# Optimization experiments

Measured on AMD Instinct MI355X. Metric: run time of the kernel, lower is better.

The kernel has to match this reference:

```python
import jax, jax.numpy as jnp
import numpy as np

NUM_INST = 3
N_NODES = 50000
IN_F = 128
HID = 64
HEADS = 4
HF = HEADS * HID  # 256
NEG_SLOPE = 0.2
BN_EPS = 1e-5


def setup_inputs() -> dict:
    key = jax.random.key(0)
    ks = jax.random.split(key, 10)
    sppmi = jax.random.normal(ks[0], (NUM_INST, N_NODES, IN_F), dtype=jnp.float32)
    edge_index = jax.random.randint(ks[1], (2, 800000), 0, N_NODES, dtype=jnp.int64)
    # Per-instance GATConv params (lin_src weight, att_src/att_dst, bias), BN, and Linear
    s = 1.0 / np.sqrt(IN_F)
    W = jax.random.uniform(ks[2], (NUM_INST, HF, IN_F), jnp.float32, -s, s)
    att_src = jax.random.uniform(ks[3], (NUM_INST, HEADS, HID), jnp.float32, -s, s)
    att_dst = jax.random.uniform(ks[4], (NUM_INST, HEADS, HID), jnp.float32, -s, s)
    bias = jnp.zeros((NUM_INST, HF), jnp.float32)
    bn_gamma = jnp.ones((NUM_INST, HF), jnp.float32)
    bn_beta = jnp.zeros((NUM_INST, HF), jnp.float32)
    bn_mean = jnp.zeros((NUM_INST, HF), jnp.float32)
    bn_var = jnp.ones((NUM_INST, HF), jnp.float32)
    s2 = 1.0 / np.sqrt(HF)
    lin_W = jax.random.uniform(ks[5], (NUM_INST, HID, HF), jnp.float32, -s2, s2)
    lin_b = jax.random.uniform(ks[6], (NUM_INST, HID), jnp.float32, -s2, s2)
    return {"sppmi": sppmi, "W": W, "att_src": att_src, "att_dst": att_dst,
            "bias": bias, "bn_gamma": bn_gamma, "bn_beta": bn_beta,
            "bn_mean": bn_mean, "bn_var": bn_var, "lin_W": lin_W,
            "lin_b": lin_b, "edge_index": edge_index}


def _gat_layer(x, W, a_src, a_dst, bias, gamma, beta, mean, var, linW, linb, src, dst):
    # GATConv (concat=True, add_self_loops already applied via src/dst)
    xw = (x @ W.T).reshape(N_NODES, HEADS, HID)            # [N,H,F]
    alpha_src = (xw * a_src).sum(-1)                        # [N,H]
    alpha_dst = (xw * a_dst).sum(-1)                        # [N,H]
    e = jax.nn.leaky_relu(alpha_src[src] + alpha_dst[dst], NEG_SLOPE)  # [E,H]
    m = jax.ops.segment_max(e, dst, num_segments=N_NODES)  # segment softmax over dst
    e = jnp.exp(e - m[dst])
    denom = jax.ops.segment_sum(e, dst, num_segments=N_NODES)
    alpha = e / (denom[dst] + 1e-16)                        # [E,H]
    msg = alpha[:, :, None] * xw[src]                       # [E,H,F] gather-attend
    out = jax.ops.segment_sum(msg, dst, num_segments=N_NODES)  # scatter-add
    out = out.reshape(N_NODES, HF) + bias
    # BatchNorm1d (eval: running stats), ReLU, Linear
    out = (out - mean) * jax.lax.rsqrt(var + BN_EPS) * gamma + beta
    out = jax.nn.relu(out)
    return out @ linW.T + linb                              # [N,HID]


def reference(sppmi, W, att_src, att_dst, bias, bn_gamma, bn_beta, bn_mean, bn_var, lin_W, lin_b, edge_index):
    loop = jnp.arange(N_NODES, dtype=edge_index.dtype)
    src = jnp.concatenate([edge_index[0], loop])
    dst = jnp.concatenate([edge_index[1], loop])
    all_emb = jnp.zeros((N_NODES, HID), jnp.float32)
    for i in range(NUM_INST):
        all_emb = all_emb + _gat_layer(sppmi[i], W[i], att_src[i], att_dst[i], bias[i],
                                       bn_gamma[i], bn_beta[i], bn_mean[i], bn_var[i],
                                       lin_W[i], lin_b[i], src, dst)
    out_1 = all_emb / jnp.linalg.norm(all_emb, axis=1, keepdims=True)
    return out_1
```

## Files before the change

kernel.cpp:

```cpp
#include <hip/hip_runtime.h>
#include <hip/hip_bf16.h>

#define N_NODES 50000
#define E0      800000
#define ET      850000
#define IN_F    128
#define HF      256
#define HID     64
#define NEG     0.2f
#define BN_EPSC 1e-5f
#define NSCAN_BLK 196

typedef __attribute__((ext_vector_type(8))) short bh8;
typedef __attribute__((ext_vector_type(4))) float fl4;
typedef __attribute__((ext_vector_type(8))) unsigned short us8;

__device__ __forceinline__ float lrelu(float x){ return x > 0.f ? x : NEG * x; }
__device__ __forceinline__ unsigned short f2b(float f){
  unsigned int x = __float_as_uint(f);
  unsigned int r = x + 0x7FFF + ((x >> 16) & 1);
  return (unsigned short)(r >> 16);
}
__device__ __forceinline__ float b2f(unsigned short u){
  return __uint_as_float((unsigned int)u << 16);
}

__global__ __launch_bounds__(256) void k_cvt(const float* __restrict__ in,
                                             unsigned short* __restrict__ out, int n4){
  int i = blockIdx.x * 256 + threadIdx.x;
  int stride = gridDim.x * 256;
  for (; i < n4; i += stride){
    float4 v = ((const float4*)in)[i];
    ushort4 o;
    o.x = f2b(v.x); o.y = f2b(v.y); o.z = f2b(v.z); o.w = f2b(v.w);
    ((ushort4*)out)[i] = o;
  }
}

__global__ __launch_bounds__(256) void k_bnprep(const float* __restrict__ g, const float* __restrict__ b,
                                                const float* __restrict__ m, const float* __restrict__ v,
                                                float* __restrict__ scale, float* __restrict__ shiftv){
  int i = blockIdx.x * 256 + threadIdx.x;
  if (i >= 3 * HF) return;
  float s = g[i] * rsqrtf(v[i] + BN_EPSC);
  scale[i] = s;
  shiftv[i] = b[i] - m[i] * s;
}

__global__ void k_hist(const int* __restrict__ ei, int* __restrict__ counts){
  int e = blockIdx.x * 256 + threadIdx.x;
  if (e >= ET) return;
  int d = (e < E0) ? ei[E0 + e] : (e - E0);
  atomicAdd(&counts[d], 1);
}

__global__ __launch_bounds__(256) void k_bsum(const int* __restrict__ counts, int* __restrict__ bsums){
  int b = blockIdx.x;
  int t = threadIdx.x;
  int idx = b * 256 + t;
  int v = (idx < N_NODES) ? counts[idx] : 0;
  for (int m = 1; m < 64; m <<= 1) v += __shfl_xor(v, m, 64);
  __shared__ int ws[4];
  int lane = t & 63, w = t >> 6;
  if (lane == 0) ws[w] = v;
  __syncthreads();
  if (t == 0) bsums[b] = ws[0] + ws[1] + ws[2] + ws[3];
}

__global__ __launch_bounds__(256) void k_bscan(const int* __restrict__ bsums, int* __restrict__ bexcl,
                                               int* __restrict__ row_ptr){
  int t = threadIdx.x;
  int v = (t < NSCAN_BLK) ? bsums[t] : 0;
  int lane = t & 63, w = t >> 6;
  int incl = v;
  for (int m = 1; m < 64; m <<= 1){
    int n = __shfl_up(incl, m, 64);
    if (lane >= m) incl += n;
  }
  __shared__ int ws[4];
  if (lane == 63) ws[w] = incl;
  __syncthreads();
  if (t == 0){
    int r = 0;
    for (int j = 0; j < 4; ++j){ int x = ws[j]; ws[j] = r; r += x; }
  }
  __syncthreads();
  int excl = incl - v + ws[w];
  if (t < NSCAN_BLK) bexcl[t] = excl;
  if (t == 255) row_ptr[N_NODES] = excl + v;
}

__global__ __launch_bounds__(256) void k_sfinal(const int* __restrict__ counts,
                                                const int* __restrict__ bexcl,
                                                int* __restrict__ row_ptr, int* __restrict__ cursor){
  int b = blockIdx.x;
  int t = threadIdx.x;
  int idx = b * 256 + t;
  int v = (idx < N_NODES) ? counts[idx] : 0;
  int lane = t & 63, w = t >> 6;
  int incl = v;
  for (int m = 1; m < 64; m <<= 1){
    int n = __shfl_up(incl, m, 64);
    if (lane >= m) incl += n;
  }
  __shared__ int ws[4];
  if (lane == 63) ws[w] = incl;
  __syncthreads();
  if (t == 0){
    int r = 0;
    for (int j = 0; j < 4; ++j){ int x = ws[j]; ws[j] = r; r += x; }
  }
  __syncthreads();
  int excl = incl - v + ws[w];
  int pos = bexcl[b] + excl;
  if (idx < N_NODES){ row_ptr[idx] = pos; cursor[idx] = pos; }
}

__global__ void k_scatter(const int* __restrict__ ei, int* __restrict__ cursor,
                          int* __restrict__ csr_src){
  int e = blockIdx.x * 256 + threadIdx.x;
  if (e >= ET) return;
  int s, d;
  if (e < E0){ s = ei[e]; d = ei[E0 + e]; } else { s = e - E0; d = s; }
  int pos = atomicAdd(&cursor[d], 1);
  csr_src[pos] = s;
}

__global__ __launch_bounds__(256) void k_gemm1f(const float* __restrict__ x,
                                                const unsigned short* __restrict__ wbv,
                                                const float* __restrict__ asrc,
                                                const float* __restrict__ adst,
                                                unsigned short* __restrict__ xwb,
                                                float* __restrict__ as_, float* __restrict__ ad_){
  __shared__ unsigned char Asm[32 * 256];
  __shared__ unsigned char Bsm[256 * 256];
  int tid = threadIdx.x;
  int m0 = blockIdx.x * 32;

  #pragma unroll
  for (int k = 0; k < 4; ++k){
    int c = k * 256 + tid;
    int row = c >> 5;
    int c4 = c & 31;
    int grow = m0 + row; if (grow >= N_NODES) grow = N_NODES - 1;
    float4 v = *(const float4*)&x[(size_t)grow * IN_F + c4 * 4];
    ushort4 o = make_ushort4(f2b(v.x), f2b(v.y), f2b(v.z), f2b(v.w));
    int colb = c4 * 8;
    int addr = row * 256 + ((colb & ~15) ^ ((row & 7) << 4)) + (colb & 15);
    *(ushort4*)(Asm + addr) = o;
  }
  #pragma unroll
  for (int k = 0; k < 16; ++k){
    int c = k * 256 + tid;
    int row = c >> 4;
    int colb = (c & 15) * 16;
    uint4 v = *(const uint4*)((const char*)wbv + (size_t)row * 256 + colb);
    *(uint4*)(Bsm + row * 256 + (colb ^ ((row & 7) << 4))) = v;
  }
  __syncthreads();

  int w = tid >> 6, lane = tid & 63;
  int l15 = lane & 15, l4 = lane >> 4;
  fl4 acc[2][4] = {};
  #pragma unroll
  for (int kk = 0; kk < 4; ++kk){
    bh8 af[2];
    #pragma unroll
    for (int m = 0; m < 2; ++m){
      int ar = m * 16 + l15;
      int ac = (kk * 64 + l4 * 16) ^ ((ar & 7) << 4);
      af[m] = *(const bh8*)(Asm + ar * 256 + ac);
    }
    bh8 bfv[4];
    #pragma unroll
    for (int n = 0; n < 4; ++n){
      int br = w * 64 + n * 16 + l15;
      int bc = (kk * 64 + l4 * 16) ^ ((br & 7) << 4);
      bfv[n] = *(const bh8*)(Bsm + br * 256 + bc);
    }
    #pragma unroll
    for (int m = 0; m < 2; ++m)
      #pragma unroll
      for (int n = 0; n < 4; ++n)
        acc[m][n] = __builtin_amdgcn_mfma_f32_16x16x32_bf16(af[m], bfv[n], acc[m][n], 0, 0, 0);
  }

  float asv[4], adv[4];
  #pragma unroll
  for (int n = 0; n < 4; ++n){
    int c = w * 64 + n * 16 + l15;
    asv[n] = asrc[c]; adv[n] = adst[c];
  }

  #pragma unroll
  for (int m = 0; m < 2; ++m){
    #pragma unroll
    for (int j = 0; j < 4; ++j){
      int grow = m0 + m * 16 + l4 * 4 + j;
      if (grow < N_NODES){
        #pragma unroll
        for (int n = 0; n < 4; ++n)
          xwb[(size_t)grow * HF + w * 64 + n * 16 + l15] = f2b(acc[m][n][j]);
      }
      float ts = acc[m][0][j]*asv[0] + acc[m][1][j]*asv[1] + acc[m][2][j]*asv[2] + acc[m][3][j]*asv[3];
      float td = acc[m][0][j]*adv[0] + acc[m][1][j]*adv[1] + acc[m][2][j]*adv[2] + acc[m][3][j]*adv[3];
      #pragma unroll
      for (int mm = 1; mm < 16; mm <<= 1){ ts += __shfl_xor(ts, mm, 64); td += __shfl_xor(td, mm, 64); }
      if (l15 == 0 && grow < N_NODES){
        as_[grow * 4 + w] = ts;
        ad_[grow * 4 + w] = td;
      }
    }
  }
}

__global__ __launch_bounds__(256) void k_agg(const unsigned short* __restrict__ xwb,
                     const float* __restrict__ as_, const float* __restrict__ ad_,
                     const int* __restrict__ row_ptr, const int* __restrict__ csr_src,
                     const float* __restrict__ bias, unsigned short* __restrict__ outb){
  __shared__ float eLds[4][4][65];
  __shared__ int   sLds[4][64];
  int w = threadIdx.x >> 6;
  int lane = threadIdx.x & 63;
  int node = blockIdx.x * 4 + w;
  int row0 = row_ptr[node];
  int deg = row_ptr[node + 1] - row0;
  float4 ad4 = *(const float4*)&ad_[node * 4];
  int h = lane >> 4;
  float accx = 0.f, accy = 0.f, accz = 0.f, accw = 0.f;
  float sh;
  const char* xwp = (const char*)xwb;
  int lb = lane * 8;

  if (deg <= 64){
    int soff = 0; float e0 = 0.f, e1 = 0.f, e2 = 0.f, e3 = 0.f;
    if (lane < deg){
      int sreg = csr_src[row0 + lane];
      soff = sreg * 512;
      float4 a4 = *(const float4*)&as_[sreg * 4];
      e0 = __expf(lrelu(a4.x + ad4.x));
      e1 = __expf(lrelu(a4.y + ad4.y));
      e2 = __expf(lrelu(a4.z + ad4.z));
      e3 = __expf(lrelu(a4.w + ad4.w));
    }
    sLds[w][lane] = soff;
    eLds[w][0][lane] = e0; eLds[w][1][lane] = e1;
    eLds[w][2][lane] = e2; eLds[w][3][lane] = e3;
    float s0 = e0, s1 = e1, s2 = e2, s3 = e3;
    for (int m = 1; m < 64; m <<= 1){
      s0 += __shfl_xor(s0, m, 64); s1 += __shfl_xor(s1, m, 64);
      s2 += __shfl_xor(s2, m, 64); s3 += __shfl_xor(s3, m, 64);
    }
    sh = (h == 0) ? s0 : (h == 1) ? s1 : (h == 2) ? s2 : s3;
    int q = 0;
    for (; q + 4 <= deg; q += 4){
      int o0 = sLds[w][q],   o1 = sLds[w][q+1];
      int o2 = sLds[w][q+2], o3 = sLds[w][q+3];
      float w0 = eLds[w][h][q],   w1 = eLds[w][h][q+1];
      float w2 = eLds[w][h][q+2], w3 = eLds[w][h][q+3];
      ushort4 u0 = *(const ushort4*)(xwp + o0 + lb);
      ushort4 u1 = *(const ushort4*)(xwp + o1 + lb);
      ushort4 u2 = *(const ushort4*)(xwp + o2 + lb);
      ushort4 u3 = *(const ushort4*)(xwp + o3 + lb);
      accx += w0*b2f(u0.x) + w1*b2f(u1.x) + w2*b2f(u2.x) + w3*b2f(u3.x);
      accy += w0*b2f(u0.y) + w1*b2f(u1.y) + w2*b2f(u2.y) + w3*b2f(u3.y);
      accz += w0*b2f(u0.z) + w1*b2f(u1.z) + w2*b2f(u2.z) + w3*b2f(u3.z);
      accw += w0*b2f(u0.w) + w1*b2f(u1.w) + w2*b2f(u2.w) + w3*b2f(u3.w);
    }
    for (; q < deg; ++q){
      int o0 = sLds[w][q];
      float wh = eLds[w][h][q];
      ushort4 u = *(const ushort4*)(xwp + o0 + lb);
      accx += wh * b2f(u.x); accy += wh * b2f(u.y);
      accz += wh * b2f(u.z); accw += wh * b2f(u.w);
    }
  } else {
    float s0 = 0.f, s1 = 0.f, s2 = 0.f, s3 = 0.f;
    for (int j = lane; j < deg; j += 64){
      int s = csr_src[row0 + j];
      float4 a4 = *(const float4*)&as_[s * 4];
      s0 += __expf(lrelu(a4.x + ad4.x));
      s1 += __expf(lrelu(a4.y + ad4.y));
      s2 += __expf(lrelu(a4.z + ad4.z));
      s3 += __expf(lrelu(a4.w + ad4.w));
    }
    for (int m = 1; m < 64; m <<= 1){
      s0 += __shfl_xor(s0, m, 64); s1 += __shfl_xor(s1, m, 64);
      s2 += __shfl_xor(s2, m, 64); s3 += __shfl_xor(s3, m, 64);
    }
    sh = (h == 0) ? s0 : (h == 1) ? s1 : (h == 2) ? s2 : s3;
    for (int jb = 0; jb < deg; jb += 64){
      int jj = jb + lane;
      int soff = 0; float e0 = 0.f, e1 = 0.f, e2 = 0.f, e3 = 0.f;
      if (jj < deg){
        int sreg = csr_src[row0 + jj];
        soff = sreg * 512;
        float4 a4 = *(const float4*)&as_[sreg * 4];
        e0 = __expf(lrelu(a4.x + ad4.x));
        e1 = __expf(lrelu(a4.y + ad4.y));
        e2 = __expf(lrelu(a4.z + ad4.z));
        e3 = __expf(lrelu(a4.w + ad4.w));
      }
      sLds[w][lane] = soff;
      eLds[w][0][lane] = e0; eLds[w][1][lane] = e1;
      eLds[w][2][lane] = e2; eLds[w][3][lane] = e3;
      __builtin_amdgcn_s_waitcnt(0);
      int lim = min(64, deg - jb);
      for (int q = 0; q < lim; ++q){
        int o0 = sLds[w][q];
        float wh = eLds[w][h][q];
        ushort4 u = *(const ushort4*)(xwp + o0 + lb);
        accx += wh * b2f(u.x); accy += wh * b2f(u.y);
        accz += wh * b2f(u.z); accw += wh * b2f(u.w);
      }
    }
  }
  float invh = 1.f / (sh + 1e-16f);
  float4 b4 = *(const float4*)&bias[lane * 4];
  ushort4 o;
  o.x = f2b(accx * invh + b4.x); o.y = f2b(accy * invh + b4.y);
  o.z = f2b(accz * invh + b4.z); o.w = f2b(accw * invh + b4.w);
  *(ushort4*)&outb[(size_t)node * HF + lane * 4] = o;
}

__global__ __launch_bounds__(256) void k_gemm2f(const unsigned short* __restrict__ ob0,
                                                const unsigned short* __restrict__ ob1,
                                                const unsigned short* __restrict__ ob2,
                                                const unsigned short* __restrict__ lwb,
                                                const float* __restrict__ scale,
                                                const float* __restrict__ shiftv,
                                                const float* __restrict__ linb,
                                                float* __restrict__ outp){
  __shared__ unsigned char Asm[64 * 512];
  __shared__ unsigned char Bsm[64 * 512];
  int tid = threadIdx.x;
  int m0 = blockIdx.x * 64;
  int w = tid >> 6, lane = tid & 63;
  int l15 = lane & 15, l4 = lane >> 4;

  fl4 acc[4] = {};
  const unsigned short* obs[3] = {ob0, ob1, ob2};

  for (int i = 0; i < 3; ++i){
    if (i) __syncthreads();
    const unsigned short* A = obs[i];
    const float* sc = scale + i * HF;
    const float* sf = shiftv + i * HF;
    #pragma unroll
    for (int k = 0; k < 8; ++k){
      int c = k * 256 + tid;
      int row = c >> 5;
      int colb = (c & 31) * 16;
      int col = colb >> 1;
      int grow = m0 + row; if (grow >= N_NODES) grow = N_NODES - 1;
      us8 u = *(const us8*)&A[(size_t)grow * HF + col];
      float4 s0 = *(const float4*)&sc[col], s1 = *(const float4*)&sc[col + 4];
      float4 f0 = *(const float4*)&sf[col], f1 = *(const float4*)&sf[col + 4];
      us8 o;
      o[0] = f2b(fmaxf(0.f, b2f(u[0]) * s0.x + f0.x));
      o[1] = f2b(fmaxf(0.f, b2f(u[1]) * s0.y + f0.y));
      o[2] = f2b(fmaxf(0.f, b2f(u[2]) * s0.z + f0.z));
      o[3] = f2b(fmaxf(0.f, b2f(u[3]) * s0.w + f0.w));
      o[4] = f2b(fmaxf(0.f, b2f(u[4]) * s1.x + f1.x));
      o[5] = f2b(fmaxf(0.f, b2f(u[5]) * s1.y + f1.y));
      o[6] = f2b(fmaxf(0.f, b2f(u[6]) * s1.z + f1.z));
      o[7] = f2b(fmaxf(0.f, b2f(u[7]) * s1.w + f1.w));
      *(us8*)(Asm + row * 512 + (colb ^ ((row & 7) << 4))) = o;
    }
    const unsigned short* B = lwb + (size_t)i * HID * HF;
    #pragma unroll
    for (int k = 0; k < 8; ++k){
      int c = k * 256 + tid;
      int row = c >> 5;
      int colb = (c & 31) * 16;
      uint4 v = *(const uint4*)((const char*)B + (size_t)row * 512 + colb);
      *(uint4*)(Bsm + row * 512 + (colb ^ ((row & 7) << 4))) = v;
    }
    __syncthreads();
    #pragma unroll
    for (int kk = 0; kk < 8; ++kk){
      int ar = w * 16 + l15;
      int ac = (kk * 64 + l4 * 16) ^ ((ar & 7) << 4);
      bh8 af = *(const bh8*)(Asm + ar * 512 + ac);
      #pragma unroll
      for (int n = 0; n < 4; ++n){
        int br = n * 16 + l15;
        int bc = (kk * 64 + l4 * 16) ^ ((br & 7) << 4);
        bh8 bfv = *(const bh8*)(Bsm + br * 512 + bc);
        acc[n] = __builtin_amdgcn_mfma_f32_16x16x32_bf16(af, bfv, acc[n], 0, 0, 0);
      }
    }
  }
  float lbs[4];
  #pragma unroll
  for (int n = 0; n < 4; ++n){
    int c = n * 16 + l15;
    lbs[n] = linb[c] + linb[64 + c] + linb[128 + c];
  }
  #pragma unroll
  for (int j = 0; j < 4; ++j){
    float v0 = acc[0][j] + lbs[0];
    float v1 = acc[1][j] + lbs[1];
    float v2 = acc[2][j] + lbs[2];
    float v3 = acc[3][j] + lbs[3];
    float ss = v0*v0 + v1*v1 + v2*v2 + v3*v3;
    #pragma unroll
    for (int mm = 1; mm < 16; mm <<= 1) ss += __shfl_xor(ss, mm, 64);
    float rn = 1.f / sqrtf(ss);
    int grow = m0 + w * 16 + l4 * 4 + j;
    if (grow < N_NODES){
      float* op = outp + (size_t)grow * HID;
      op[l15]      = v0 * rn;
      op[16 + l15] = v1 * rn;
      op[32 + l15] = v2 * rn;
      op[48 + l15] = v3 * rn;
    }
  }
}

extern "C" void kernel_launch(void* const* d_in, const int* in_sizes, int n_in,
                              void* d_out, int out_size, void* d_ws, size_t ws_size,
                              hipStream_t stream){
  const float* sppmi   = (const float*)d_in[0];
  const float* W       = (const float*)d_in[1];
  const float* att_src = (const float*)d_in[2];
  const float* att_dst = (const float*)d_in[3];
  const float* bias    = (const float*)d_in[4];
  const float* bn_g    = (const float*)d_in[5];
  const float* bn_b    = (const float*)d_in[6];
  const float* bn_m    = (const float*)d_in[7];
  const float* bn_v    = (const float*)d_in[8];
  const float* lin_W   = (const float*)d_in[9];
  const float* lin_b   = (const float*)d_in[10];
  const int*   ei      = (const int*)d_in[11];

  char* ws = (char*)d_ws;
  size_t off = 0;
  auto alloc = [&](size_t bytes)->char*{ char* p = ws + off; off += (bytes + 255) & ~(size_t)255; return p; };
  unsigned short* wb   = (unsigned short*)alloc((size_t)3 * HF * IN_F * 2);
  unsigned short* lwb  = (unsigned short*)alloc((size_t)3 * HID * HF * 2);
  float* scale  = (float*)alloc((size_t)3 * HF * 4);
  float* shiftv = (float*)alloc((size_t)3 * HF * 4);
  unsigned short* xwb  = (unsigned short*)alloc((size_t)N_NODES * HF * 2);
  unsigned short* outb0 = (unsigned short*)alloc((size_t)N_NODES * HF * 2);
  unsigned short* outb1 = (unsigned short*)alloc((size_t)N_NODES * HF * 2);
  unsigned short* outb2 = (unsigned short*)alloc((size_t)N_NODES * HF * 2);
  float* as_    = (float*)alloc((size_t)N_NODES * 4 * 4);
  float* ad_    = (float*)alloc((size_t)N_NODES * 4 * 4);
  int* counts   = (int*)alloc((size_t)N_NODES * 4);
  int* row_ptr  = (int*)alloc((size_t)(N_NODES + 4) * 4);
  int* cursor   = (int*)alloc((size_t)N_NODES * 4);
  int* csr      = (int*)alloc((size_t)ET * 4);
  int* bsums    = (int*)alloc((size_t)NSCAN_BLK * 4);
  int* bexcl    = (int*)alloc((size_t)NSCAN_BLK * 4);
  unsigned short* obs[3] = {outb0, outb1, outb2};

  hipMemsetAsync(counts, 0, (size_t)N_NODES * 4, stream);

  k_cvt<<<96, 256, 0, stream>>>(W, wb, 3 * HF * IN_F / 4);
  k_cvt<<<48, 256, 0, stream>>>(lin_W, lwb, 3 * HID * HF / 4);
  k_bnprep<<<3, 256, 0, stream>>>(bn_g, bn_b, bn_m, bn_v, scale, shiftv);

  k_hist<<<(ET + 255) / 256, 256, 0, stream>>>(ei, counts);
  k_bsum<<<NSCAN_BLK, 256, 0, stream>>>(counts, bsums);
  k_bscan<<<1, 256, 0, stream>>>(bsums, bexcl, row_ptr);
  k_sfinal<<<NSCAN_BLK, 256, 0, stream>>>(counts, bexcl, row_ptr, cursor);
  k_scatter<<<(ET + 255) / 256, 256, 0, stream>>>(ei, cursor, csr);

  for (int i = 0; i < 3; ++i){
    k_gemm1f<<<1563, 256, 0, stream>>>(sppmi + (size_t)i * N_NODES * IN_F,
                                       wb + (size_t)i * HF * IN_F,
                                       att_src + i * HF, att_dst + i * HF,
                                       xwb, as_, ad_);
    k_agg<<<12500, 256, 0, stream>>>(xwb, as_, ad_, row_ptr, csr, bias + i * HF, obs[i]);
  }
  k_gemm2f<<<782, 256, 0, stream>>>(outb0, outb1, outb2, lwb, scale, shiftv,
                                    (const float*)d_in[10], (float*)d_out);
}
```

Before: 399.2 us.

## Batch all instances per launch and split XW into per-half-head planes for aggregation

Merges the three per-instance GEMM1 and aggregation launches into single launches, and merges the weight-conversion and BN-prep kernels into one prep kernel. GEMM1 now writes XW as two 128-column planes (heads 0-1 and heads 2-3) per instance. The aggregation kernel handles one half per block, so each gathered source row is 256 bytes instead of 512, which shrinks the gather working set and improves L2 reuse. In exchange the edge list and softmax exponentials are read and computed twice per node, and the three instances' buffers must all be live at once, which uses more memory.

```diff
diff --git a/kernel.cpp b/kernel.cpp
--- a/kernel.cpp
+++ b/kernel.cpp
@@ -10,6 +10,7 @@
 #define NEG     0.2f
 #define BN_EPSC 1e-5f
 #define NSCAN_BLK 196
+#define HALF_F  128
 
 typedef __attribute__((ext_vector_type(8))) short bh8;
 typedef __attribute__((ext_vector_type(4))) float fl4;
@@ -25,26 +26,27 @@
   return __uint_as_float((unsigned int)u << 16);
 }
 
-__global__ __launch_bounds__(256) void k_cvt(const float* __restrict__ in,
-                                             unsigned short* __restrict__ out, int n4){
-  int i = blockIdx.x * 256 + threadIdx.x;
-  int stride = gridDim.x * 256;
-  for (; i < n4; i += stride){
-    float4 v = ((const float4*)in)[i];
-    ushort4 o;
-    o.x = f2b(v.x); o.y = f2b(v.y); o.z = f2b(v.z); o.w = f2b(v.w);
-    ((ushort4*)out)[i] = o;
-  }
-}
-
-__global__ __launch_bounds__(256) void k_bnprep(const float* __restrict__ g, const float* __restrict__ b,
-                                                const float* __restrict__ m, const float* __restrict__ v,
-                                                float* __restrict__ scale, float* __restrict__ shiftv){
-  int i = blockIdx.x * 256 + threadIdx.x;
-  if (i >= 3 * HF) return;
-  float s = g[i] * rsqrtf(v[i] + BN_EPSC);
-  scale[i] = s;
-  shiftv[i] = b[i] - m[i] * s;
+#define NW4 (3 * HF * IN_F / 4)
+#define NL4 (3 * HID * HF / 4)
+__global__ __launch_bounds__(256) void k_prep(const float* __restrict__ W, unsigned short* __restrict__ wb,
+                                              const float* __restrict__ linW, unsigned short* __restrict__ lwb,
+                                              const float* __restrict__ g, const float* __restrict__ b,
+                                              const float* __restrict__ m, const float* __restrict__ v,
+                                              float* __restrict__ scale, float* __restrict__ shiftv){
+  int idx = blockIdx.x * 256 + threadIdx.x;
+  if (idx < NW4){
+    float4 x = ((const float4*)W)[idx];
+    ((ushort4*)wb)[idx] = make_ushort4(f2b(x.x), f2b(x.y), f2b(x.z), f2b(x.w));
+  } else if (idx < NW4 + NL4){
+    int j = idx - NW4;
+    float4 x = ((const float4*)linW)[j];
+    ((ushort4*)lwb)[j] = make_ushort4(f2b(x.x), f2b(x.y), f2b(x.z), f2b(x.w));
+  } else if (idx < NW4 + NL4 + 3 * HF){
+    int i = idx - NW4 - NL4;
+    float s = g[i] * rsqrtf(v[i] + BN_EPSC);
+    scale[i] = s;
+    shiftv[i] = b[i] - m[i] * s;
+  }
 }
 
 __global__ void k_hist(const int* __restrict__ ei, int* __restrict__ counts){
@@ -126,16 +128,24 @@
   csr_src[pos] = s;
 }
 
-__global__ __launch_bounds__(256) void k_gemm1f(const float* __restrict__ x,
-                                                const unsigned short* __restrict__ wbv,
-                                                const float* __restrict__ asrc,
-                                                const float* __restrict__ adst,
-                                                unsigned short* __restrict__ xwb,
-                                                float* __restrict__ as_, float* __restrict__ ad_){
+__global__ __launch_bounds__(256) void k_gemm1f(const float* __restrict__ sppmi,
+                                                const unsigned short* __restrict__ wb,
+                                                const float* __restrict__ att_src,
+                                                const float* __restrict__ att_dst,
+                                                unsigned short* __restrict__ xw3,
+                                                float* __restrict__ as3, float* __restrict__ ad3){
   __shared__ unsigned char Asm[32 * 256];
   __shared__ unsigned char Bsm[256 * 256];
   int tid = threadIdx.x;
-  int m0 = blockIdx.x * 32;
+  int bx = blockIdx.x;
+  int inst = bx / 1563;
+  int m0 = (bx % 1563) * 32;
+  const float* x = sppmi + (size_t)inst * N_NODES * IN_F;
+  const unsigned short* wbv = wb + (size_t)inst * HF * IN_F;
+  const float* asrc = att_src + inst * HF;
+  const float* adst = att_dst + inst * HF;
+  float* as_ = as3 + (size_t)inst * N_NODES * 4;
+  float* ad_ = ad3 + (size_t)inst * N_NODES * 4;
 
   #pragma unroll
   for (int k = 0; k < 4; ++k){
@@ -192,6 +202,9 @@
     asv[n] = asrc[c]; adv[n] = adst[c];
   }
 
+  unsigned short* xwh = xw3 + ((size_t)inst * 2 + (w >> 1)) * (size_t)N_NODES * HALF_F;
+  int cbase = (w & 1) * 64;
+
   #pragma unroll
   for (int m = 0; m < 2; ++m){
     #pragma unroll
@@ -200,7 +213,7 @@
       if (grow < N_NODES){
         #pragma unroll
         for (int n = 0; n < 4; ++n)
-          xwb[(size_t)grow * HF + w * 64 + n * 16 + l15] = f2b(acc[m][n][j]);
+          xwh[(size_t)grow * HALF_F + cbase + n * 16 + l15] = f2b(acc[m][n][j]);
       }
       float ts = acc[m][0][j]*asv[0] + acc[m][1][j]*asv[1] + acc[m][2][j]*asv[2] + acc[m][3][j]*asv[3];
       float td = acc[m][0][j]*adv[0] + acc[m][1][j]*adv[1] + acc[m][2][j]*adv[2] + acc[m][3][j]*adv[3];
@@ -214,118 +227,114 @@
   }
 }
 
-__global__ __launch_bounds__(256) void k_agg(const unsigned short* __restrict__ xwb,
-                     const float* __restrict__ as_, const float* __restrict__ ad_,
+__global__ __launch_bounds__(256) void k_agg3(const unsigned short* __restrict__ xw3,
+                     const float* __restrict__ as3, const float* __restrict__ ad3,
                      const int* __restrict__ row_ptr, const int* __restrict__ csr_src,
                      const float* __restrict__ bias, unsigned short* __restrict__ outb){
-  __shared__ float eLds[4][4][65];
+  __shared__ float eLds[4][2][65];
   __shared__ int   sLds[4][64];
+  int bx = blockIdx.x;
+  int inst = bx / 25000;
+  int rem = bx - inst * 25000;
+  int half = (rem >> 2) & 1;
+  int chunk = (rem >> 3) * 4 + (rem & 3);
   int w = threadIdx.x >> 6;
   int lane = threadIdx.x & 63;
-  int node = blockIdx.x * 4 + w;
+  int node = chunk * 4 + w;
   int row0 = row_ptr[node];
   int deg = row_ptr[node + 1] - row0;
-  float4 ad4 = *(const float4*)&ad_[node * 4];
-  int h = lane >> 4;
-  float accx = 0.f, accy = 0.f, accz = 0.f, accw = 0.f;
+  const float* as_ = as3 + (size_t)inst * N_NODES * 4;
+  const float* ad_ = ad3 + (size_t)inst * N_NODES * 4;
+  float2 ad2 = *(const float2*)&ad_[node * 4 + half * 2];
+  int head = lane >> 5;
+  const char* xwp = (const char*)(xw3 + ((size_t)inst * 2 + half) * (size_t)N_NODES * HALF_F);
+  int lb = lane * 4;
+  float accx = 0.f, accy = 0.f;
   float sh;
-  const char* xwp = (const char*)xwb;
-  int lb = lane * 8;
 
   if (deg <= 64){
-    int soff = 0; float e0 = 0.f, e1 = 0.f, e2 = 0.f, e3 = 0.f;
+    int soff = 0; float e0 = 0.f, e1 = 0.f;
     if (lane < deg){
       int sreg = csr_src[row0 + lane];
-      soff = sreg * 512;
-      float4 a4 = *(const float4*)&as_[sreg * 4];
-      e0 = __expf(lrelu(a4.x + ad4.x));
-      e1 = __expf(lrelu(a4.y + ad4.y));
-      e2 = __expf(lrelu(a4.z + ad4.z));
-      e3 = __expf(lrelu(a4.w + ad4.w));
+      soff = sreg << 8;
+      float2 a2 = *(const float2*)&as_[sreg * 4 + half * 2];
+      e0 = __expf(lrelu(a2.x + ad2.x));
+      e1 = __expf(lrelu(a2.y + ad2.y));
     }
     sLds[w][lane] = soff;
     eLds[w][0][lane] = e0; eLds[w][1][lane] = e1;
-    eLds[w][2][lane] = e2; eLds[w][3][lane] = e3;
-    float s0 = e0, s1 = e1, s2 = e2, s3 = e3;
+    float s0 = e0, s1 = e1;
     for (int m = 1; m < 64; m <<= 1){
       s0 += __shfl_xor(s0, m, 64); s1 += __shfl_xor(s1, m, 64);
-      s2 += __shfl_xor(s2, m, 64); s3 += __shfl_xor(s3, m, 64);
-    }
-    sh = (h == 0) ? s0 : (h == 1) ? s1 : (h == 2) ? s2 : s3;
+    }
+    sh = head ? s1 : s0;
     int q = 0;
     for (; q + 4 <= deg; q += 4){
       int o0 = sLds[w][q],   o1 = sLds[w][q+1];
       int o2 = sLds[w][q+2], o3 = sLds[w][q+3];
-      float w0 = eLds[w][h][q],   w1 = eLds[w][h][q+1];
-      float w2 = eLds[w][h][q+2], w3 = eLds[w][h][q+3];
-      ushort4 u0 = *(const ushort4*)(xwp + o0 + lb);
-      ushort4 u1 = *(const ushort4*)(xwp + o1 + lb);
-      ushort4 u2 = *(const ushort4*)(xwp + o2 + lb);
-      ushort4 u3 = *(const ushort4*)(xwp + o3 + lb);
-      accx += w0*b2f(u0.x) + w1*b2f(u1.x) + w2*b2f(u2.x) + w3*b2f(u3.x);
-      accy += w0*b2f(u0.y) + w1*b2f(u1.y) + w2*b2f(u2.y) + w3*b2f(u3.y);
-      accz += w0*b2f(u0.z) + w1*b2f(u1.z) + w2*b2f(u2.z) + w3*b2f(u3.z);
-      accw += w0*b2f(u0.w) + w1*b2f(u1.w) + w2*b2f(u2.w) + w3*b2f(u3.w);
+      float w0 = eLds[w][head][q],   w1 = eLds[w][head][q+1];
+      float w2 = eLds[w][head][q+2], w3 = eLds[w][head][q+3];
+      unsigned int u0 = *(const unsigned int*)(xwp + o0 + lb);
+      unsigned int u1 = *(const unsigned int*)(xwp + o1 + lb);
+      unsigned int u2 = *(const unsigned int*)(xwp + o2 + lb);
+      unsigned int u3 = *(const unsigned int*)(xwp + o3 + lb);
+      accx += w0*__uint_as_float(u0 << 16) + w1*__uint_as_float(u1 << 16)
+            + w2*__uint_as_float(u2 << 16) + w3*__uint_as_float(u3 << 16);
+      accy += w0*__uint_as_float(u0 & 0xffff0000u) + w1*__uint_as_float(u1 & 0xffff0000u)
+            + w2*__uint_as_float(u2 & 0xffff0000u) + w3*__uint_as_float(u3 & 0xffff0000u);
     }
     for (; q < deg; ++q){
       int o0 = sLds[w][q];
-      float wh = eLds[w][h][q];
-      ushort4 u = *(const ushort4*)(xwp + o0 + lb);
-      accx += wh * b2f(u.x); accy += wh * b2f(u.y);
-      accz += wh * b2f(u.z); accw += wh * b2f(u.w);
+      float wh = eLds[w][head][q];
+      unsigned int u = *(const unsigned int*)(xwp + o0 + lb);
+      accx += wh * __uint_as_float(u << 16);
+      accy += wh * __uint_as_float(u & 0xffff0000u);
     }
   } else {
-    float s0 = 0.f, s1 = 0.f, s2 = 0.f, s3 = 0.f;
+    float s0 = 0.f, s1 = 0.f;
     for (int j = lane; j < deg; j += 64){
       int s = csr_src[row0 + j];
-      float4 a4 = *(const float4*)&as_[s * 4];
-      s0 += __expf(lrelu(a4.x + ad4.x));
-      s1 += __expf(lrelu(a4.y + ad4.y));
-      s2 += __expf(lrelu(a4.z + ad4.z));
-      s3 += __expf(lrelu(a4.w + ad4.w));
+      float2 a2 = *(const float2*)&as_[s * 4 + half * 2];
+      s0 += __expf(lrelu(a2.x + ad2.x));
+      s1 += __expf(lrelu(a2.y + ad2.y));
     }
     for (int m = 1; m < 64; m <<= 1){
       s0 += __shfl_xor(s0, m, 64); s1 += __shfl_xor(s1, m, 64);
-      s2 += __shfl_xor(s2, m, 64); s3 += __shfl_xor(s3, m, 64);
-    }
-    sh = (h == 0) ? s0 : (h == 1) ? s1 : (h == 2) ? s2 : s3;
+    }
+    sh = head ? s1 : s0;
     for (int jb = 0; jb < deg; jb += 64){
       int jj = jb + lane;
-      int soff = 0; float e0 = 0.f, e1 = 0.f, e2 = 0.f, e3 = 0.f;
+      int soff = 0; float e0 = 0.f, e1 = 0.f;
       if (jj < deg){
         int sreg = csr_src[row0 + jj];
-        soff = sreg * 512;
-        float4 a4 = *(const float4*)&as_[sreg * 4];
-        e0 = __expf(lrelu(a4.x + ad4.x));
-        e1 = __expf(lrelu(a4.y + ad4.y));
-        e2 = __expf(lrelu(a4.z + ad4.z));
-        e3 = __expf(lrelu(a4.w + ad4.w));
+        soff = sreg << 8;
+        float2 a2 = *(const float2*)&as_[sreg * 4 + half * 2];
+        e0 = __expf(lrelu(a2.x + ad2.x));
+        e1 = __expf(lrelu(a2.y + ad2.y));
       }
       sLds[w][lane] = soff;
       eLds[w][0][lane] = e0; eLds[w][1][lane] = e1;
-      eLds[w][2][lane] = e2; eLds[w][3][lane] = e3;
       __builtin_amdgcn_s_waitcnt(0);
       int lim = min(64, deg - jb);
       for (int q = 0; q < lim; ++q){
         int o0 = sLds[w][q];
-        float wh = eLds[w][h][q];
-        ushort4 u = *(const ushort4*)(xwp + o0 + lb);
-        accx += wh * b2f(u.x); accy += wh * b2f(u.y);
-        accz += wh * b2f(u.z); accw += wh * b2f(u.w);
+        float wh = eLds[w][head][q];
+        unsigned int u = *(const unsigned int*)(xwp + o0 + lb);
+        accx += wh * __uint_as_float(u << 16);
+        accy += wh * __uint_as_float(u & 0xffff0000u);
       }
     }
   }
   float invh = 1.f / (sh + 1e-16f);
-  float4 b4 = *(const float4*)&bias[lane * 4];
-  ushort4 o;
-  o.x = f2b(accx * invh + b4.x); o.y = f2b(accy * invh + b4.y);
-  o.z = f2b(accz * invh + b4.z); o.w = f2b(accw * invh + b4.w);
-  *(ushort4*)&outb[(size_t)node * HF + lane * 4] = o;
-}
-
-__global__ __launch_bounds__(256) void k_gemm2f(const unsigned short* __restrict__ ob0,
-                                                const unsigned short* __restrict__ ob1,
-                                                const unsigned short* __restrict__ ob2,
+  int col = half * HALF_F + lane * 2;
+  float b0 = bias[inst * HF + col], b1 = bias[inst * HF + col + 1];
+  ushort2 o;
+  o.x = f2b(accx * invh + b0);
+  o.y = f2b(accy * invh + b1);
+  *(ushort2*)&outb[(size_t)inst * N_NODES * HF + (size_t)node * HF + col] = o;
+}
+
+__global__ __launch_bounds__(256) void k_gemm2f(const unsigned short* __restrict__ obase,
                                                 const unsigned short* __restrict__ lwb,
                                                 const float* __restrict__ scale,
                                                 const float* __restrict__ shiftv,
@@ -339,11 +348,10 @@
   int l15 = lane & 15, l4 = lane >> 4;
 
   fl4 acc[4] = {};
-  const unsigned short* obs[3] = {ob0, ob1, ob2};
 
   for (int i = 0; i < 3; ++i){
     if (i) __syncthreads();
-    const unsigned short* A = obs[i];
+    const unsigned short* A = obase + (size_t)i * N_NODES * HF;
     const float* sc = scale + i * HF;
     const float* sf = shiftv + i * HF;
     #pragma unroll
@@ -441,25 +449,20 @@
   unsigned short* lwb  = (unsigned short*)alloc((size_t)3 * HID * HF * 2);
   float* scale  = (float*)alloc((size_t)3 * HF * 4);
   float* shiftv = (float*)alloc((size_t)3 * HF * 4);
-  unsigned short* xwb  = (unsigned short*)alloc((size_t)N_NODES * HF * 2);
-  unsigned short* outb0 = (unsigned short*)alloc((size_t)N_NODES * HF * 2);
-  unsigned short* outb1 = (unsigned short*)alloc((size_t)N_NODES * HF * 2);
-  unsigned short* outb2 = (unsigned short*)alloc((size_t)N_NODES * HF * 2);
-  float* as_    = (float*)alloc((size_t)N_NODES * 4 * 4);
-  float* ad_    = (float*)alloc((size_t)N_NODES * 4 * 4);
+  unsigned short* xw3  = (unsigned short*)alloc((size_t)3 * 2 * N_NODES * HALF_F * 2);
+  unsigned short* outb = (unsigned short*)alloc((size_t)3 * N_NODES * HF * 2);
+  float* as3    = (float*)alloc((size_t)3 * N_NODES * 4 * 4);
+  float* ad3    = (float*)alloc((size_t)3 * N_NODES * 4 * 4);
   int* counts   = (int*)alloc((size_t)N_NODES * 4);
   int* row_ptr  = (int*)alloc((size_t)(N_NODES + 4) * 4);
   int* cursor   = (int*)alloc((size_t)N_NODES * 4);
   int* csr      = (int*)alloc((size_t)ET * 4);
   int* bsums    = (int*)alloc((size_t)NSCAN_BLK * 4);
   int* bexcl    = (int*)alloc((size_t)NSCAN_BLK * 4);
-  unsigned short* obs[3] = {outb0, outb1, outb2};
 
   hipMemsetAsync(counts, 0, (size_t)N_NODES * 4, stream);
 
-  k_cvt<<<96, 256, 0, stream>>>(W, wb, 3 * HF * IN_F / 4);
-  k_cvt<<<48, 256, 0, stream>>>(lin_W, lwb, 3 * HID * HF / 4);
-  k_bnprep<<<3, 256, 0, stream>>>(bn_g, bn_b, bn_m, bn_v, scale, shiftv);
+  k_prep<<<147, 256, 0, stream>>>(W, wb, lin_W, lwb, bn_g, bn_b, bn_m, bn_v, scale, shiftv);
 
   k_hist<<<(ET + 255) / 256, 256, 0, stream>>>(ei, counts);
   k_bsum<<<NSCAN_BLK, 256, 0, stream>>>(counts, bsums);
@@ -467,13 +470,7 @@
   k_sfinal<<<NSCAN_BLK, 256, 0, stream>>>(counts, bexcl, row_ptr, cursor);
   k_scatter<<<(ET + 255) / 256, 256, 0, stream>>>(ei, cursor, csr);
 
-  for (int i = 0; i < 3; ++i){
-    k_gemm1f<<<1563, 256, 0, stream>>>(sppmi + (size_t)i * N_NODES * IN_F,
-                                       wb + (size_t)i * HF * IN_F,
-                                       att_src + i * HF, att_dst + i * HF,
-                                       xwb, as_, ad_);
-    k_agg<<<12500, 256, 0, stream>>>(xwb, as_, ad_, row_ptr, csr, bias + i * HF, obs[i]);
-  }
-  k_gemm2f<<<782, 256, 0, stream>>>(outb0, outb1, outb2, lwb, scale, shiftv,
-                                    (const float*)d_in[10], (float*)d_out);
-}
+  k_gemm1f<<<3 * 1563, 256, 0, stream>>>(sppmi, wb, att_src, att_dst, xw3, as3, ad3);
+  k_agg3<<<75000, 256, 0, stream>>>(xw3, as3, ad3, row_ptr, csr, bias, outb);
+  k_gemm2f<<<782, 256, 0, stream>>>(outb, lwb, scale, shiftv, lin_b, (float*)d_out);
+}
```

After: 373.1 us. -6.6%, faster.

## Batch three GAT instances into single launches and load weights directly from global

Applied to the files above, without the earlier changes.

Fuses the three weight-conversion and BN prep kernels into one prep kernel. Batches the per-instance gemm1 and aggregation launches into single grids covering all three instances, using per-instance xw and attention buffers. Doubles the gemm1 M tile to 64 rows, and in both GEMMs drops the LDS staging of B so fragments load directly from global/L2. The aim is fewer launches, a larger grid and less LDS traffic, at the cost of more workspace memory and uncoalesced B reads from global.

```diff
diff --git a/kernel.cpp b/kernel.cpp
--- a/kernel.cpp
+++ b/kernel.cpp
@@ -25,26 +25,27 @@
   return __uint_as_float((unsigned int)u << 16);
 }
 
-__global__ __launch_bounds__(256) void k_cvt(const float* __restrict__ in,
-                                             unsigned short* __restrict__ out, int n4){
-  int i = blockIdx.x * 256 + threadIdx.x;
-  int stride = gridDim.x * 256;
-  for (; i < n4; i += stride){
-    float4 v = ((const float4*)in)[i];
-    ushort4 o;
-    o.x = f2b(v.x); o.y = f2b(v.y); o.z = f2b(v.z); o.w = f2b(v.w);
-    ((ushort4*)out)[i] = o;
-  }
-}
-
-__global__ __launch_bounds__(256) void k_bnprep(const float* __restrict__ g, const float* __restrict__ b,
-                                                const float* __restrict__ m, const float* __restrict__ v,
-                                                float* __restrict__ scale, float* __restrict__ shiftv){
-  int i = blockIdx.x * 256 + threadIdx.x;
-  if (i >= 3 * HF) return;
-  float s = g[i] * rsqrtf(v[i] + BN_EPSC);
-  scale[i] = s;
-  shiftv[i] = b[i] - m[i] * s;
+#define NW4 (3 * HF * IN_F / 4)
+#define NL4 (3 * HID * HF / 4)
+__global__ __launch_bounds__(256) void k_prep(const float* __restrict__ W, unsigned short* __restrict__ wb,
+                                              const float* __restrict__ linW, unsigned short* __restrict__ lwb,
+                                              const float* __restrict__ g, const float* __restrict__ b,
+                                              const float* __restrict__ m, const float* __restrict__ v,
+                                              float* __restrict__ scale, float* __restrict__ shiftv){
+  int idx = blockIdx.x * 256 + threadIdx.x;
+  if (idx < NW4){
+    float4 x = ((const float4*)W)[idx];
+    ((ushort4*)wb)[idx] = make_ushort4(f2b(x.x), f2b(x.y), f2b(x.z), f2b(x.w));
+  } else if (idx < NW4 + NL4){
+    int j = idx - NW4;
+    float4 x = ((const float4*)linW)[j];
+    ((ushort4*)lwb)[j] = make_ushort4(f2b(x.x), f2b(x.y), f2b(x.z), f2b(x.w));
+  } else if (idx < NW4 + NL4 + 3 * HF){
+    int i = idx - NW4 - NL4;
+    float s = g[i] * rsqrtf(v[i] + BN_EPSC);
+    scale[i] = s;
+    shiftv[i] = b[i] - m[i] * s;
+  }
 }
 
 __global__ void k_hist(const int* __restrict__ ei, int* __restrict__ counts){
@@ -126,19 +127,27 @@
   csr_src[pos] = s;
 }
 
-__global__ __launch_bounds__(256) void k_gemm1f(const float* __restrict__ x,
-                                                const unsigned short* __restrict__ wbv,
-                                                const float* __restrict__ asrc,
-                                                const float* __restrict__ adst,
+__global__ __launch_bounds__(256) void k_gemm1f(const float* __restrict__ sppmi,
+                                                const unsigned short* __restrict__ wb,
+                                                const float* __restrict__ att_src,
+                                                const float* __restrict__ att_dst,
                                                 unsigned short* __restrict__ xwb,
-                                                float* __restrict__ as_, float* __restrict__ ad_){
-  __shared__ unsigned char Asm[32 * 256];
-  __shared__ unsigned char Bsm[256 * 256];
+                                                float* __restrict__ as3, float* __restrict__ ad3){
+  __shared__ unsigned char Asm[64 * 256];
   int tid = threadIdx.x;
-  int m0 = blockIdx.x * 32;
-
-  #pragma unroll
-  for (int k = 0; k < 4; ++k){
+  int bx = blockIdx.x;
+  int inst = bx / 782;
+  int m0 = (bx % 782) * 64;
+  const float* x = sppmi + (size_t)inst * N_NODES * IN_F;
+  const unsigned short* wbv = wb + (size_t)inst * HF * IN_F;
+  const float* asrc = att_src + inst * HF;
+  const float* adst = att_dst + inst * HF;
+  float* as_ = as3 + (size_t)inst * N_NODES * 4;
+  float* ad_ = ad3 + (size_t)inst * N_NODES * 4;
+  unsigned short* xw = xwb + (size_t)inst * N_NODES * HF;
+
+  #pragma unroll
+  for (int k = 0; k < 8; ++k){
     int c = k * 256 + tid;
     int row = c >> 5;
     int c4 = c & 31;
@@ -149,37 +158,27 @@
     int addr = row * 256 + ((colb & ~15) ^ ((row & 7) << 4)) + (colb & 15);
     *(ushort4*)(Asm + addr) = o;
   }
-  #pragma unroll
-  for (int k = 0; k < 16; ++k){
-    int c = k * 256 + tid;
-    int row = c >> 4;
-    int colb = (c & 15) * 16;
-    uint4 v = *(const uint4*)((const char*)wbv + (size_t)row * 256 + colb);
-    *(uint4*)(Bsm + row * 256 + (colb ^ ((row & 7) << 4))) = v;
-  }
   __syncthreads();
 
   int w = tid >> 6, lane = tid & 63;
   int l15 = lane & 15, l4 = lane >> 4;
-  fl4 acc[2][4] = {};
+  const char* bbase = (const char*)wbv + (size_t)(w * 64 + l15) * 256 + l4 * 16;
+  fl4 acc[4][4] = {};
   #pragma unroll
   for (int kk = 0; kk < 4; ++kk){
-    bh8 af[2];
-    #pragma unroll
-    for (int m = 0; m < 2; ++m){
+    bh8 bfv[4];
+    #pragma unroll
+    for (int n = 0; n < 4; ++n)
+      bfv[n] = *(const bh8*)(bbase + n * 16 * 256 + kk * 64);
+    bh8 af[4];
+    #pragma unroll
+    for (int m = 0; m < 4; ++m){
       int ar = m * 16 + l15;
       int ac = (kk * 64 + l4 * 16) ^ ((ar & 7) << 4);
       af[m] = *(const bh8*)(Asm + ar * 256 + ac);
     }
-    bh8 bfv[4];
-    #pragma unroll
-    for (int n = 0; n < 4; ++n){
-      int br = w * 64 + n * 16 + l15;
-      int bc = (kk * 64 + l4 * 16) ^ ((br & 7) << 4);
-      bfv[n] = *(const bh8*)(Bsm + br * 256 + bc);
-    }
-    #pragma unroll
-    for (int m = 0; m < 2; ++m)
+    #pragma unroll
+    for (int m = 0; m < 4; ++m)
       #pragma unroll
       for (int n = 0; n < 4; ++n)
         acc[m][n] = __builtin_amdgcn_mfma_f32_16x16x32_bf16(af[m], bfv[n], acc[m][n], 0, 0, 0);
@@ -193,14 +192,14 @@
   }
 
   #pragma unroll
-  for (int m = 0; m < 2; ++m){
+  for (int m = 0; m < 4; ++m){
     #pragma unroll
     for (int j = 0; j < 4; ++j){
       int grow = m0 + m * 16 + l4 * 4 + j;
       if (grow < N_NODES){
         #pragma unroll
         for (int n = 0; n < 4; ++n)
-          xwb[(size_t)grow * HF + w * 64 + n * 16 + l15] = f2b(acc[m][n][j]);
+          xw[(size_t)grow * HF + w * 64 + n * 16 + l15] = f2b(acc[m][n][j]);
       }
       float ts = acc[m][0][j]*asv[0] + acc[m][1][j]*asv[1] + acc[m][2][j]*asv[2] + acc[m][3][j]*asv[3];
       float td = acc[m][0][j]*adv[0] + acc[m][1][j]*adv[1] + acc[m][2][j]*adv[2] + acc[m][3][j]*adv[3];
@@ -214,22 +213,27 @@
   }
 }
 
-__global__ __launch_bounds__(256) void k_agg(const unsigned short* __restrict__ xwb,
-                     const float* __restrict__ as_, const float* __restrict__ ad_,
+__global__ __launch_bounds__(256) void k_agg3(const unsigned short* __restrict__ xwb,
+                     const float* __restrict__ as3, const float* __restrict__ ad3,
                      const int* __restrict__ row_ptr, const int* __restrict__ csr_src,
                      const float* __restrict__ bias, unsigned short* __restrict__ outb){
   __shared__ float eLds[4][4][65];
   __shared__ int   sLds[4][64];
+  int bx = blockIdx.x;
+  int inst = bx / 12500;
+  int chunk = bx - inst * 12500;
   int w = threadIdx.x >> 6;
   int lane = threadIdx.x & 63;
-  int node = blockIdx.x * 4 + w;
+  int node = chunk * 4 + w;
   int row0 = row_ptr[node];
   int deg = row_ptr[node + 1] - row0;
+  const float* as_ = as3 + (size_t)inst * N_NODES * 4;
+  const float* ad_ = ad3 + (size_t)inst * N_NODES * 4;
   float4 ad4 = *(const float4*)&ad_[node * 4];
   int h = lane >> 4;
   float accx = 0.f, accy = 0.f, accz = 0.f, accw = 0.f;
   float sh;
-  const char* xwp = (const char*)xwb;
+  const char* xwp = (const char*)(xwb + (size_t)inst * N_NODES * HF);
   int lb = lane * 8;
 
   if (deg <= 64){
@@ -316,34 +320,31 @@
     }
   }
   float invh = 1.f / (sh + 1e-16f);
-  float4 b4 = *(const float4*)&bias[lane * 4];
+  const float* bi = bias + inst * HF;
+  float4 b4 = *(const float4*)&bi[lane * 4];
   ushort4 o;
   o.x = f2b(accx * invh + b4.x); o.y = f2b(accy * invh + b4.y);
   o.z = f2b(accz * invh + b4.z); o.w = f2b(accw * invh + b4.w);
-  *(ushort4*)&outb[(size_t)node * HF + lane * 4] = o;
-}
-
-__global__ __launch_bounds__(256) void k_gemm2f(const unsigned short* __restrict__ ob0,
-                                                const unsigned short* __restrict__ ob1,
-                                                const unsigned short* __restrict__ ob2,
+  *(ushort4*)&outb[(size_t)inst * N_NODES * HF + (size_t)node * HF + lane * 4] = o;
+}
+
+__global__ __launch_bounds__(256) void k_gemm2f(const unsigned short* __restrict__ obase,
                                                 const unsigned short* __restrict__ lwb,
                                                 const float* __restrict__ scale,
                                                 const float* __restrict__ shiftv,
                                                 const float* __restrict__ linb,
                                                 float* __restrict__ outp){
   __shared__ unsigned char Asm[64 * 512];
-  __shared__ unsigned char Bsm[64 * 512];
   int tid = threadIdx.x;
   int m0 = blockIdx.x * 64;
   int w = tid >> 6, lane = tid & 63;
   int l15 = lane & 15, l4 = lane >> 4;
 
   fl4 acc[4] = {};
-  const unsigned short* obs[3] = {ob0, ob1, ob2};
 
   for (int i = 0; i < 3; ++i){
     if (i) __syncthreads();
-    const unsigned short* A = obs[i];
+    const unsigned short* A = obase + (size_t)i * N_NODES * HF;
     const float* sc = scale + i * HF;
     const float* sf = shiftv + i * HF;
     #pragma unroll
@@ -367,16 +368,8 @@
       o[7] = f2b(fmaxf(0.f, b2f(u[7]) * s1.w + f1.w));
       *(us8*)(Asm + row * 512 + (colb ^ ((row & 7) << 4))) = o;
     }
-    const unsigned short* B = lwb + (size_t)i * HID * HF;
-    #pragma unroll
-    for (int k = 0; k < 8; ++k){
-      int c = k * 256 + tid;
-      int row = c >> 5;
-      int colb = (c & 31) * 16;
-      uint4 v = *(const uint4*)((const char*)B + (size_t)row * 512 + colb);
-      *(uint4*)(Bsm + row * 512 + (colb ^ ((row & 7) << 4))) = v;
-    }
     __syncthreads();
+    const char* bbase = (const char*)(lwb + (size_t)i * HID * HF) + (size_t)l15 * 512 + l4 * 16;
     #pragma unroll
     for (int kk = 0; kk < 8; ++kk){
       int ar = w * 16 + l15;
@@ -384,9 +377,7 @@
       bh8 af = *(const bh8*)(Asm + ar * 512 + ac);
       #pragma unroll
       for (int n = 0; n < 4; ++n){
-        int br = n * 16 + l15;
-        int bc = (kk * 64 + l4 * 16) ^ ((br & 7) << 4);
-        bh8 bfv = *(const bh8*)(Bsm + br * 512 + bc);
+        bh8 bfv = *(const bh8*)(bbase + n * 16 * 512 + kk * 64);
         acc[n] = __builtin_amdgcn_mfma_f32_16x16x32_bf16(af, bfv, acc[n], 0, 0, 0);
       }
     }
@@ -441,25 +432,20 @@
   unsigned short* lwb  = (unsigned short*)alloc((size_t)3 * HID * HF * 2);
   float* scale  = (float*)alloc((size_t)3 * HF * 4);
   float* shiftv = (float*)alloc((size_t)3 * HF * 4);
-  unsigned short* xwb  = (unsigned short*)alloc((size_t)N_NODES * HF * 2);
-  unsigned short* outb0 = (unsigned short*)alloc((size_t)N_NODES * HF * 2);
-  unsigned short* outb1 = (unsigned short*)alloc((size_t)N_NODES * HF * 2);
-  unsigned short* outb2 = (unsigned short*)alloc((size_t)N_NODES * HF * 2);
-  float* as_    = (float*)alloc((size_t)N_NODES * 4 * 4);
-  float* ad_    = (float*)alloc((size_t)N_NODES * 4 * 4);
+  unsigned short* xwb  = (unsigned short*)alloc((size_t)3 * N_NODES * HF * 2);
+  unsigned short* outb = (unsigned short*)alloc((size_t)3 * N_NODES * HF * 2);
+  float* as3    = (float*)alloc((size_t)3 * N_NODES * 4 * 4);
+  float* ad3    = (float*)alloc((size_t)3 * N_NODES * 4 * 4);
   int* counts   = (int*)alloc((size_t)N_NODES * 4);
   int* row_ptr  = (int*)alloc((size_t)(N_NODES + 4) * 4);
   int* cursor   = (int*)alloc((size_t)N_NODES * 4);
   int* csr      = (int*)alloc((size_t)ET * 4);
   int* bsums    = (int*)alloc((size_t)NSCAN_BLK * 4);
   int* bexcl    = (int*)alloc((size_t)NSCAN_BLK * 4);
-  unsigned short* obs[3] = {outb0, outb1, outb2};
 
   hipMemsetAsync(counts, 0, (size_t)N_NODES * 4, stream);
 
-  k_cvt<<<96, 256, 0, stream>>>(W, wb, 3 * HF * IN_F / 4);
-  k_cvt<<<48, 256, 0, stream>>>(lin_W, lwb, 3 * HID * HF / 4);
-  k_bnprep<<<3, 256, 0, stream>>>(bn_g, bn_b, bn_m, bn_v, scale, shiftv);
+  k_prep<<<147, 256, 0, stream>>>(W, wb, lin_W, lwb, bn_g, bn_b, bn_m, bn_v, scale, shiftv);
 
   k_hist<<<(ET + 255) / 256, 256, 0, stream>>>(ei, counts);
   k_bsum<<<NSCAN_BLK, 256, 0, stream>>>(counts, bsums);
@@ -467,13 +453,7 @@
   k_sfinal<<<NSCAN_BLK, 256, 0, stream>>>(counts, bexcl, row_ptr, cursor);
   k_scatter<<<(ET + 255) / 256, 256, 0, stream>>>(ei, cursor, csr);
 
-  for (int i = 0; i < 3; ++i){
-    k_gemm1f<<<1563, 256, 0, stream>>>(sppmi + (size_t)i * N_NODES * IN_F,
-                                       wb + (size_t)i * HF * IN_F,
-                                       att_src + i * HF, att_dst + i * HF,
-                                       xwb, as_, ad_);
-    k_agg<<<12500, 256, 0, stream>>>(xwb, as_, ad_, row_ptr, csr, bias + i * HF, obs[i]);
-  }
-  k_gemm2f<<<782, 256, 0, stream>>>(outb0, outb1, outb2, lwb, scale, shiftv,
-                                    (const float*)d_in[10], (float*)d_out);
-}
+  k_gemm1f<<<3 * 782, 256, 0, stream>>>(sppmi, wb, att_src, att_dst, xwb, as3, ad3);
+  k_agg3<<<37500, 256, 0, stream>>>(xwb, as3, ad3, row_ptr, csr, bias, outb);
+  k_gemm2f<<<782, 256, 0, stream>>>(outb, lwb, scale, shiftv, lin_b, (float*)d_out);
+}
```

Result: no change. 393.7 us (-1.4%).
